# Performance work log

Hardware: AMD Instinct MI355X
Metric: run time of the kernel (lower is better)

Reference implementation:

```python
import jax, jax.numpy as jnp
import numpy as np

B, N, QD = 2, 1024, 512          # batch (ref+feat), tokens (32x32), query_dim
H, DH = 8, 64                    # heads, dim_head
INNER = H * DH
HW = 64                          # raw mask spatial size
SCALE = DH ** (-0.5)


def setup_inputs() -> dict:
    key = jax.random.key(0)
    ks = jax.random.split(key, 6)
    s = 0.02
    x = jax.random.normal(ks[0], (B, N, QD), jnp.float32)
    mask = jax.random.randint(ks[1], (B // 2, 1, HW, HW), 0, 2).astype(jnp.float32)
    Wq = jax.random.normal(ks[2], (INNER, QD), jnp.float32) * s
    Wk = jax.random.normal(ks[3], (INNER, QD), jnp.float32) * s
    Wv = jax.random.normal(ks[4], (INNER, QD), jnp.float32) * s
    # zero_module only zeroes to_out at init; use random weights for a meaningful baseline
    Wo = jax.random.normal(ks[5], (QD, INNER), jnp.float32) * s
    bo = jnp.zeros((QD,), jnp.float32)
    return {"x": x, "mask": mask, "Wq": Wq, "Wk": Wk, "Wv": Wv, "Wo": Wo, "bo": bo, "share": 1}


def nearest_resize(m, size):
    # PyTorch F.interpolate(mode='nearest'): src = floor(dst * in/out)
    ih = (jnp.arange(size) * m.shape[-2]) // size
    iw = (jnp.arange(size) * m.shape[-1]) // size
    return m[:, :, ih][:, :, :, iw]


def adain(feat, ref, mask):
    # feat, ref: (b, n, d); mask: (b, n, 1) binary
    ref_std = jnp.std(ref, axis=-2, keepdims=True, ddof=1)   # torch std is unbiased
    ref_mean = jnp.mean(ref, axis=-2, keepdims=True)
    cnt = jnp.sum(mask, axis=-2, keepdims=True)              # (b,1,1)
    f_mean = jnp.sum(feat * mask, axis=-2, keepdims=True) / cnt
    f_var = jnp.sum(mask * (feat - f_mean) ** 2, axis=-2, keepdims=True) / (cnt - 1.0)
    f_std = jnp.sqrt(f_var)
    new = (feat - f_mean) / f_std * ref_std + ref_mean
    return new * mask + feat * (1.0 - mask)


def split_heads(t):
    b, n, _ = t.shape
    return t.reshape(b, n, H, DH).transpose(0, 2, 1, 3).reshape(b * H, n, DH)


def reference(x, mask, Wq, Wk, Wv, Wo, bo, share):
    q = x @ Wq.T
    k = x @ Wk.T
    v = x @ Wv.T
    size = int(N ** 0.5)  # 32
    m = nearest_resize(mask, size).reshape(-1, N, 1)  # (B//2, N, 1)
    ref_k, feat_k = k[: B // 2], k[B // 2:]
    ref_v, feat_v = v[: B // 2], v[B // 2:]
    feat_k = adain(feat_k, ref_k, m)
    feat_v = adain(feat_v, ref_v, m)
    k = jnp.concatenate([ref_k, feat_k], axis=0)
    v = jnp.concatenate([ref_v, feat_v], axis=0)
    k = jnp.concatenate([k, jnp.tile(ref_k, (2, 1, 1))], axis=1)  # (B, 2N, INNER)
    v = jnp.concatenate([v, jnp.tile(ref_v, (2, 1, 1))], axis=1)
    qh, kh, vh = split_heads(q), split_heads(k), split_heads(v)
    sim = jnp.einsum('bid,bjd->bij', qh, kh) * SCALE  # (B*H, N, 2N)
    am = jnp.tile(m, (H, 1, N))                       # (B//2*H, N, N)
    am = (1.0 - am) * (-1e9)
    am = jnp.concatenate([jnp.zeros_like(am), am], axis=0)   # (B*H, N, N)
    am = jnp.concatenate([jnp.zeros_like(am), am], axis=-1)  # (B*H, N, 2N)
    attn = jax.nn.softmax(sim + am, axis=-1)
    out = jnp.einsum('bij,bjd->bid', attn, vh)               # (B*H, N, DH)
    out = out.reshape(B, H, N, DH).transpose(0, 2, 1, 3).reshape(B, N, INNER)
    return out @ Wo.T + bo
```

## Files before the change

### kernel.cpp

```cpp
#include <hip/hip_runtime.h>
#include <math.h>

#define NTOK 1024
#define QDIM 512
#define NH 8
#define DHD 64

using s16x8 = __attribute__((ext_vector_type(8))) short;
using f32x4 = __attribute__((ext_vector_type(4))) float;

__device__ __forceinline__ unsigned short f2bf(float x) {
  union { float f; unsigned u; } v; v.f = x;
  unsigned r = (v.u + 0x7fffu + ((v.u >> 16) & 1u)) >> 16;
  return (unsigned short)r;
}
__device__ __forceinline__ float bf2f(unsigned short h) {
  union { unsigned u; float f; } v; v.u = ((unsigned)h) << 16;
  return v.f;
}
__device__ __forceinline__ unsigned cvt_pk_bf16(float lo, float hi) {
  unsigned r;
  asm volatile("v_cvt_pk_bf16_f32 %0, %1, %2" : "=v"(r) : "v"(lo), "v"(hi));
  return r;
}

__global__ __launch_bounds__(256) void cast_kernel(
    const float* __restrict__ x, const float* __restrict__ Wq, const float* __restrict__ Wk,
    const float* __restrict__ Wv, const float* __restrict__ Wo, unsigned short* __restrict__ dst)
{
  const int tid = blockIdx.x * 256 + threadIdx.x;
  const int e = tid * 4;
  const float* src;
  if (e < 1048576) {
    src = x + e;
  } else {
    const int we = e - 1048576;
    const int wi = we >> 18;
    const int off = we & 262143;
    src = (wi == 0 ? Wq : wi == 1 ? Wk : wi == 2 ? Wv : Wo) + off;
  }
  float4 v = *(const float4*)src;
  ushort4 o;
  o.x = f2bf(v.x); o.y = f2bf(v.y); o.z = f2bf(v.z); o.w = f2bf(v.w);
  *(ushort4*)&dst[e] = o;
}

__global__ __launch_bounds__(256) void proj_mfma_kernel(
    const unsigned short* __restrict__ x_b, const unsigned short* __restrict__ w_b,
    unsigned short* __restrict__ q_b, unsigned short* __restrict__ k_b,
    unsigned short* __restrict__ v_b)
{
  const int w = threadIdx.x >> 6;
  const int l = threadIdx.x & 63;
  const int lq = l & 15, lg = l >> 4;
  const int tile = blockIdx.x * 4 + w;
  const int mat = blockIdx.y >> 3;
  const int h = blockIdx.y & 7;
  const unsigned short* W = w_b + (size_t)mat * 262144 + (size_t)(h * 64) * QDIM;
  const int tok0 = tile * 16;

  const unsigned short* xp = &x_b[(size_t)(tok0 + lq) * QDIM + lg * 8];
  const unsigned short* wp = &W[(size_t)lq * QDIM + lg * 8];

  f32x4 acc[4] = {};
  s16x8 aA, bA[4], aB, bB[4];
  aA = *(const s16x8*)&xp[0];
#pragma unroll
  for (int nf = 0; nf < 4; ++nf) bA[nf] = *(const s16x8*)&wp[(size_t)nf * 16 * QDIM];

  for (int kt = 0; kt < 16; kt += 2) {
    aB = *(const s16x8*)&xp[(kt + 1) * 32];
#pragma unroll
    for (int nf = 0; nf < 4; ++nf) bB[nf] = *(const s16x8*)&wp[(size_t)nf * 16 * QDIM + (kt + 1) * 32];
#pragma unroll
    for (int nf = 0; nf < 4; ++nf)
      acc[nf] = __builtin_amdgcn_mfma_f32_16x16x32_bf16(aA, bA[nf], acc[nf], 0, 0, 0);
    if (kt + 2 < 16) {
      aA = *(const s16x8*)&xp[(kt + 2) * 32];
#pragma unroll
      for (int nf = 0; nf < 4; ++nf) bA[nf] = *(const s16x8*)&wp[(size_t)nf * 16 * QDIM + (kt + 2) * 32];
    }
#pragma unroll
    for (int nf = 0; nf < 4; ++nf)
      acc[nf] = __builtin_amdgcn_mfma_f32_16x16x32_bf16(aB, bB[nf], acc[nf], 0, 0, 0);
  }

  const float scale = (mat == 0) ? 0.125f : 1.0f;
  unsigned short* dst = (mat == 0 ? q_b : mat == 1 ? k_b : v_b);
  const int b = tok0 >> 10;
  const int tl0 = tok0 & 1023;
  unsigned short* dp = dst + (size_t)(b * NH + h) * NTOK * DHD;
#pragma unroll
  for (int nf = 0; nf < 4; ++nf)
#pragma unroll
    for (int r = 0; r < 4; ++r)
      dp[(size_t)(tl0 + lg * 4 + r) * DHD + nf * 16 + lq] = f2bf(acc[nf][r] * scale);
}

__global__ __launch_bounds__(256) void adain_stats_kernel(
    const unsigned short* __restrict__ k_b, const unsigned short* __restrict__ v_b,
    const float* __restrict__ mask, float* __restrict__ stats_p, float* __restrict__ stats_cnt)
{
  const int id = blockIdx.x;
  const int arr = id >> 7, h = (id >> 4) & 7, ch = id & 15;
  const unsigned short* base = arr ? v_b : k_b;
  const unsigned short* refp = base + (size_t)h * 65536;
  const unsigned short* fep  = base + (size_t)(8 + h) * 65536;
  const int t = threadIdx.x, dh = t & 63, ig = t >> 6;

  if (arr == 0 && h == 0 && t < 64) {
    const int tok = ch * 64 + t;
    float c = mask[(tok >> 5) * 128 + (tok & 31) * 2];
#pragma unroll
    for (int off = 1; off < 64; off <<= 1) c += __shfl_xor(c, off);
    if (t == 0) stats_cnt[ch] = c;
  }

  float rs = 0.f, rq = 0.f, fs = 0.f, fq = 0.f;
  for (int i = 0; i < 16; ++i) {
    const int tok = ch * 64 + ig * 16 + i;
    const float rv = bf2f(refp[(size_t)tok * DHD + dh]);
    rs += rv; rq += rv * rv;
    const float fv = bf2f(fep[(size_t)tok * DHD + dh]);
    const float mm = mask[(tok >> 5) * 128 + (tok & 31) * 2];
    fs += mm * fv; fq += mm * fv * fv;
  }
  __shared__ float red[4][256];
  red[0][t] = rs; red[1][t] = rq; red[2][t] = fs; red[3][t] = fq;
  __syncthreads();
  if (ig == 0) {
    rs = red[0][dh] + red[0][dh + 64] + red[0][dh + 128] + red[0][dh + 192];
    rq = red[1][dh] + red[1][dh + 64] + red[1][dh + 128] + red[1][dh + 192];
    fs = red[2][dh] + red[2][dh + 64] + red[2][dh + 128] + red[2][dh + 192];
    fq = red[3][dh] + red[3][dh + 64] + red[3][dh + 128] + red[3][dh + 192];
    float* sp = stats_p + (size_t)id * 256;
    sp[dh] = rs; sp[64 + dh] = rq; sp[128 + dh] = fs; sp[192 + dh] = fq;
  }
}

__global__ __launch_bounds__(256) void adain_apply_kernel(
    unsigned short* __restrict__ k_b, unsigned short* __restrict__ v_b,
    const float* __restrict__ mask, const float* __restrict__ stats_p,
    const float* __restrict__ stats_cnt)
{
  const int id = blockIdx.x;
  const int arr = id >> 7, h = (id >> 4) & 7, ch = id & 15;
  unsigned short* fep = (arr ? v_b : k_b) + (size_t)(8 + h) * 65536;
  const int t = threadIdx.x, dh = t & 63, ig = t >> 6;

  __shared__ float sA[64], sB[64];
  if (t < 64) {
    float cnt = 0.f;
#pragma unroll
    for (int c = 0; c < 16; ++c) cnt += stats_cnt[c];
    const float* sp = stats_p + (size_t)((arr << 7) | (h << 4)) * 256;
    float rs = 0.f, rq = 0.f, fs = 0.f, fq = 0.f;
#pragma unroll
    for (int c = 0; c < 16; ++c) {
      rs += sp[c * 256 + t]; rq += sp[c * 256 + 64 + t];
      fs += sp[c * 256 + 128 + t]; fq += sp[c * 256 + 192 + t];
    }
    const float rmean = rs * (1.0f / 1024.0f);
    const float rstd = sqrtf(fmaxf((rq - 1024.0f * rmean * rmean) * (1.0f / 1023.0f), 0.f));
    const float fmean = fs / cnt;
    const float fstd = sqrtf(fmaxf((fq - cnt * fmean * fmean) / (cnt - 1.0f), 0.f));
    const float a = rstd / fstd;
    sA[t] = a; sB[t] = rmean - fmean * a;
  }
  __syncthreads();
  const float a = sA[dh], bb = sB[dh];
  for (int i = 0; i < 16; ++i) {
    const int tok = ch * 64 + ig * 16 + i;
    if (mask[(tok >> 5) * 128 + (tok & 31) * 2] != 0.f) {
      const float fv = bf2f(fep[(size_t)tok * DHD + dh]);
      fep[(size_t)tok * DHD + dh] = f2bf(fv * a + bb);
    }
  }
}

__global__ __launch_bounds__(256) void vtrans_kernel(const unsigned short* __restrict__ v_b,
                                                     unsigned short* __restrict__ v_bT)
{
  const int bh = blockIdx.y;
  const int tc = blockIdx.x;
  __shared__ unsigned short T[64][72];
  const int t = threadIdx.x;
  {
    const int tok = t >> 2, d0 = (t & 3) * 16;
    const unsigned short* src = v_b + ((size_t)bh * NTOK + tc * 64 + tok) * DHD + d0;
    ushort4 a0 = *(const ushort4*)&src[0];
    ushort4 a1 = *(const ushort4*)&src[4];
    ushort4 a2 = *(const ushort4*)&src[8];
    ushort4 a3 = *(const ushort4*)&src[12];
    T[d0 + 0][tok] = a0.x; T[d0 + 1][tok] = a0.y; T[d0 + 2][tok] = a0.z; T[d0 + 3][tok] = a0.w;
    T[d0 + 4][tok] = a1.x; T[d0 + 5][tok] = a1.y; T[d0 + 6][tok] = a1.z; T[d0 + 7][tok] = a1.w;
    T[d0 + 8][tok] = a2.x; T[d0 + 9][tok] = a2.y; T[d0 +10][tok] = a2.z; T[d0 +11][tok] = a2.w;
    T[d0 +12][tok] = a3.x; T[d0 +13][tok] = a3.y; T[d0 +14][tok] = a3.z; T[d0 +15][tok] = a3.w;
  }
  __syncthreads();
  {
    const int dh = t >> 2, t0 = (t & 3) * 16;
    unsigned short* dst = v_bT + ((size_t)bh * DHD + dh) * NTOK + tc * 64 + t0;
    s16x8 r0 = *(const s16x8*)&T[dh][t0];
    s16x8 r1 = *(const s16x8*)&T[dh][t0 + 8];
    *(s16x8*)&dst[0] = r0;
    *(s16x8*)&dst[8] = r1;
  }
}

__global__ __launch_bounds__(256, 4) void attn_part_kernel(
    const unsigned short* __restrict__ q_b, const unsigned short* __restrict__ k_b,
    const unsigned short* __restrict__ v_bT, const float* __restrict__ mask,
    unsigned short* __restrict__ pO, float* __restrict__ pml)
{
  const int w = threadIdx.x >> 6;
  const int unit = blockIdx.x * 4 + w;
  int b, rr;
  if (unit < 2048) { b = 1; rr = unit; } else { b = 0; rr = unit - 2048; }
  const int hh = rr >> 8;
  const int qb = (rr >> 3) & 31;
  const int s  = rr & 7;
  const int bh = b * 8 + hh;
  const int l = threadIdx.x & 63, lq = l & 15, lg = l >> 4;

  __shared__ unsigned int P_u[4][2][16][36];

  const unsigned short* qbase = q_b + ((size_t)bh * NTOK + qb * 32) * DHD;
  s16x8 qfA0 = *(const s16x8*)&qbase[(size_t)lq * DHD + lg * 8];
  s16x8 qfA1 = *(const s16x8*)&qbase[(size_t)lq * DHD + 32 + lg * 8];
  s16x8 qfB0 = *(const s16x8*)&qbase[(size_t)(16 + lq) * DHD + lg * 8];
  s16x8 qfB1 = *(const s16x8*)&qbase[(size_t)(16 + lq) * DHD + 32 + lg * 8];

  const int ntile = (b == 0) ? 2 : 4;
  const int kv0 = s * ntile * 64;
  const int inref = (b == 1 && kv0 >= NTOK) ? 1 : 0;
  const int off0 = inref ? (kv0 - NTOK) : kv0;
  const size_t base = (size_t)(inref ? hh : bh) * 65536;
  const unsigned short* kbase = k_b + base + (size_t)off0 * DHD;
  const unsigned short* vbase = v_bT + base + off0;

  float mnegA = 0.f, mnegB = 0.f;
  if (inref) {
    const int qA = qb * 32 + lq, qB = qA + 16;
    mnegA = (1.0f - mask[(qA >> 5) * 128 + (qA & 31) * 2]) * (-1e9f);
    mnegB = (1.0f - mask[(qB >> 5) * 128 + (qB & 31) * 2]) * (-1e9f);
  }

  float mrowA = -1e30f, lrowA = 0.f;
  float mrowB = -1e30f, lrowB = 0.f;
  f32x4 oA[4] = {}, oB[4] = {};

  for (int tt = 0; tt < ntile; ++tt) {
    const unsigned short* kp = kbase + (size_t)tt * 64 * DHD;
    const unsigned short* vp = vbase + tt * 64;

    f32x4 sfA[4], sfB[4];
#pragma unroll
    for (int mf = 0; mf < 4; ++mf) {
      s16x8 a0 = *(const s16x8*)&kp[(size_t)(mf * 16 + lq) * DHD + lg * 8];
      s16x8 a1 = *(const s16x8*)&kp[(size_t)(mf * 16 + lq) * DHD + 32 + lg * 8];
      f32x4 z0 = {};
      z0 = __builtin_amdgcn_mfma_f32_16x16x32_bf16(a0, qfA0, z0, 0, 0, 0);
      sfA[mf] = __builtin_amdgcn_mfma_f32_16x16x32_bf16(a1, qfA1, z0, 0, 0, 0);
      f32x4 z1 = {};
      z1 = __builtin_amdgcn_mfma_f32_16x16x32_bf16(a0, qfB0, z1, 0, 0, 0);
      sfB[mf] = __builtin_amdgcn_mfma_f32_16x16x32_bf16(a1, qfB1, z1, 0, 0, 0);
    }

    const float addA = inref ? mnegA : 0.0f;
    const float addB = inref ? mnegB : 0.0f;
    float tmA = -1e30f, tmB = -1e30f;
#pragma unroll
    for (int mf = 0; mf < 4; ++mf)
#pragma unroll
      for (int r = 0; r < 4; ++r) {
        sfA[mf][r] += addA; tmA = fmaxf(tmA, sfA[mf][r]);
        sfB[mf][r] += addB; tmB = fmaxf(tmB, sfB[mf][r]);
      }
    tmA = fmaxf(tmA, __shfl_xor(tmA, 16));
    tmA = fmaxf(tmA, __shfl_xor(tmA, 32));
    tmB = fmaxf(tmB, __shfl_xor(tmB, 16));
    tmB = fmaxf(tmB, __shfl_xor(tmB, 32));

    if (!__all(tmA <= mrowA + 8.0f)) {
      const float mnew = fmaxf(mrowA, tmA);
      const float alpha = __expf(mrowA - mnew);
      mrowA = mnew;
      lrowA *= alpha;
      float ar[4];
#pragma unroll
      for (int r = 0; r < 4; ++r) ar[r] = __shfl(alpha, lg * 4 + r, 16);
#pragma unroll
      for (int nf = 0; nf < 4; ++nf)
#pragma unroll
        for (int r = 0; r < 4; ++r) oA[nf][r] *= ar[r];
    }
    if (!__all(tmB <= mrowB + 8.0f)) {
      const float mnew = fmaxf(mrowB, tmB);
      const float alpha = __expf(mrowB - mnew);
      mrowB = mnew;
      lrowB *= alpha;
      float ar[4];
#pragma unroll
      for (int r = 0; r < 4; ++r) ar[r] = __shfl(alpha, lg * 4 + r, 16);
#pragma unroll
      for (int nf = 0; nf < 4; ++nf)
#pragma unroll
        for (int r = 0; r < 4; ++r) oB[nf][r] *= ar[r];
    }

    float pA[4][4], pB[4][4];
    float psA = 0.f, psB = 0.f;
#pragma unroll
    for (int mf = 0; mf < 4; ++mf)
#pragma unroll
      for (int r = 0; r < 4; ++r) {
        const float eA = __expf(sfA[mf][r] - mrowA); pA[mf][r] = eA; psA += eA;
        const float eB = __expf(sfB[mf][r] - mrowB); pB[mf][r] = eB; psB += eB;
      }
    psA += __shfl_xor(psA, 16);
    psA += __shfl_xor(psA, 32);
    lrowA += psA;
    psB += __shfl_xor(psB, 16);
    psB += __shfl_xor(psB, 32);
    lrowB += psB;

#pragma unroll
    for (int mf = 0; mf < 4; ++mf) {
      uint2 wa;
      wa.x = cvt_pk_bf16(pA[mf][0], pA[mf][1]);
      wa.y = cvt_pk_bf16(pA[mf][2], pA[mf][3]);
      *(uint2*)&P_u[w][0][lq][8 * mf + 2 * lg] = wa;
      uint2 wb;
      wb.x = cvt_pk_bf16(pB[mf][0], pB[mf][1]);
      wb.y = cvt_pk_bf16(pB[mf][2], pB[mf][3]);
      *(uint2*)&P_u[w][1][lq][8 * mf + 2 * lg] = wb;
    }

#pragma unroll
    for (int ks = 0; ks < 2; ++ks) {
      s16x8 paA = *(const s16x8*)&P_u[w][0][lq][16 * ks + 4 * lg];
      s16x8 paB = *(const s16x8*)&P_u[w][1][lq][16 * ks + 4 * lg];
#pragma unroll
      for (int nf = 0; nf < 4; ++nf) {
        s16x8 vb = *(const s16x8*)&vp[(size_t)(nf * 16 + lq) * NTOK + ks * 32 + lg * 8];
        oA[nf] = __builtin_amdgcn_mfma_f32_16x16x32_bf16(paA, vb, oA[nf], 0, 0, 0);
        oB[nf] = __builtin_amdgcn_mfma_f32_16x16x32_bf16(paB, vb, oB[nf], 0, 0, 0);
      }
    }
  }

  const int u = (bh * 32 + qb) * 8 + s;
  unsigned short* pop = pO + (size_t)u * 2048;
#pragma unroll
  for (int nf = 0; nf < 4; ++nf)
#pragma unroll
    for (int r = 0; r < 4; ++r) {
      pop[(size_t)(lg * 4 + r) * DHD + nf * 16 + lq] = f2bf(oA[nf][r]);
      pop[(size_t)(16 + lg * 4 + r) * DHD + nf * 16 + lq] = f2bf(oB[nf][r]);
    }
  if (l < 16) {
    pml[(size_t)u * 64 + lq] = mrowA;
    pml[(size_t)u * 64 + 16 + lq] = lrowA;
  } else if (l < 32) {
    pml[(size_t)u * 64 + 32 + lq] = mrowB;
    pml[(size_t)u * 64 + 48 + lq] = lrowB;
  }
}

__global__ __launch_bounds__(64) void attn_merge_kernel(
    const unsigned short* __restrict__ pO, const float* __restrict__ pml,
    unsigned short* __restrict__ o_b)
{
  const int id = blockIdx.x;
  const int bh = id >> 6, qt = id & 63;
  const int qb = qt >> 1, half = qt & 1;
  const int l = threadIdx.x, r = l & 15, dblk = l >> 4;
  const int d0 = dblk * 16;
  const int u0 = (bh * 32 + qb) * 8;
  const int mo = half * 32;
  const int row = half * 16 + r;

  float ms[8], ls[8];
  float M = -1e30f;
#pragma unroll
  for (int s = 0; s < 8; ++s) {
    ms[s] = pml[(size_t)(u0 + s) * 64 + mo + r];
    ls[s] = pml[(size_t)(u0 + s) * 64 + mo + 16 + r];
    M = fmaxf(M, ms[s]);
  }
  float Lsum = 0.f;
  float o[16];
#pragma unroll
  for (int j = 0; j < 16; ++j) o[j] = 0.f;
#pragma unroll
  for (int s = 0; s < 8; ++s) {
    const float alpha = __expf(ms[s] - M);
    Lsum += alpha * ls[s];
    const unsigned short* po = pO + (size_t)(u0 + s) * 2048 + (size_t)row * DHD + d0;
    s16x8 a = *(const s16x8*)&po[0];
    s16x8 c = *(const s16x8*)&po[8];
#pragma unroll
    for (int j = 0; j < 8; ++j) {
      o[j] += alpha * bf2f((unsigned short)a[j]);
      o[8 + j] += alpha * bf2f((unsigned short)c[j]);
    }
  }
  const float inv = 1.0f / Lsum;
  unsigned short* dst = o_b + ((size_t)bh * NTOK + qt * 16 + r) * DHD + d0;
  ushort4 w0, w1, w2, w3;
  w0.x = f2bf(o[0] * inv);  w0.y = f2bf(o[1] * inv);  w0.z = f2bf(o[2] * inv);  w0.w = f2bf(o[3] * inv);
  w1.x = f2bf(o[4] * inv);  w1.y = f2bf(o[5] * inv);  w1.z = f2bf(o[6] * inv);  w1.w = f2bf(o[7] * inv);
  w2.x = f2bf(o[8] * inv);  w2.y = f2bf(o[9] * inv);  w2.z = f2bf(o[10] * inv); w2.w = f2bf(o[11] * inv);
  w3.x = f2bf(o[12] * inv); w3.y = f2bf(o[13] * inv); w3.z = f2bf(o[14] * inv); w3.w = f2bf(o[15] * inv);
  *(ushort4*)&dst[0] = w0; *(ushort4*)&dst[4] = w1;
  *(ushort4*)&dst[8] = w2; *(ushort4*)&dst[12] = w3;
}

__global__ __launch_bounds__(256) void outproj_mfma_kernel(
    const unsigned short* __restrict__ o_b, const unsigned short* __restrict__ Wo_b,
    const float* __restrict__ bo, float* __restrict__ out)
{
  const int w = threadIdx.x >> 6, l = threadIdx.x & 63;
  const int lq = l & 15, lg = l >> 4;
  const int tile = blockIdx.x * 4 + w;
  const int c0 = blockIdx.y * 64;
  const int tok = tile * 16 + lq;
  const int b = tok >> 10, tl = tok & 1023;

  const unsigned short* obase = o_b + (size_t)(b * NH) * NTOK * DHD + (size_t)tl * DHD + lg * 8;
  const unsigned short* wp = &Wo_b[(size_t)(c0 + lq) * QDIM + lg * 8];

#define OP_A(KT) (*(const s16x8*)&obase[(size_t)((KT) >> 1) * NTOK * DHD + ((KT) & 1) * 32])

  f32x4 acc[4] = {};
  s16x8 aA, bA[4], aB, bB[4];
  aA = OP_A(0);
#pragma unroll
  for (int nf = 0; nf < 4; ++nf) bA[nf] = *(const s16x8*)&wp[(size_t)nf * 16 * QDIM];

  for (int kt = 0; kt < 16; kt += 2) {
    aB = OP_A(kt + 1);
#pragma unroll
    for (int nf = 0; nf < 4; ++nf) bB[nf] = *(const s16x8*)&wp[(size_t)nf * 16 * QDIM + (kt + 1) * 32];
#pragma unroll
    for (int nf = 0; nf < 4; ++nf)
      acc[nf] = __builtin_amdgcn_mfma_f32_16x16x32_bf16(aA, bA[nf], acc[nf], 0, 0, 0);
    if (kt + 2 < 16) {
      aA = OP_A(kt + 2);
#pragma unroll
      for (int nf = 0; nf < 4; ++nf) bA[nf] = *(const s16x8*)&wp[(size_t)nf * 16 * QDIM + (kt + 2) * 32];
    }
#pragma unroll
    for (int nf = 0; nf < 4; ++nf)
      acc[nf] = __builtin_amdgcn_mfma_f32_16x16x32_bf16(aB, bB[nf], acc[nf], 0, 0, 0);
  }
#undef OP_A

  const int row0 = tile * 16;
#pragma unroll
  for (int nf = 0; nf < 4; ++nf) {
    const float bv = bo[c0 + nf * 16 + lq];
#pragma unroll
    for (int r = 0; r < 4; ++r)
      out[(size_t)(row0 + lg * 4 + r) * QDIM + c0 + nf * 16 + lq] = acc[nf][r] + bv;
  }
}

extern "C" void kernel_launch(void* const* d_in, const int* in_sizes, int n_in,
                              void* d_out, int out_size, void* d_ws, size_t ws_size,
                              hipStream_t stream) {
  const float* x    = (const float*)d_in[0];
  const float* mask = (const float*)d_in[1];
  const float* Wq   = (const float*)d_in[2];
  const float* Wk   = (const float*)d_in[3];
  const float* Wv   = (const float*)d_in[4];
  const float* Wo   = (const float*)d_in[5];
  const float* bo   = (const float*)d_in[6];
  float* out = (float*)d_out;

  char* ws = (char*)d_ws;
  unsigned short* x_b  = (unsigned short*)ws;
  unsigned short* w_b  = (unsigned short*)(ws + 2097152);
  unsigned short* Wo_b = (unsigned short*)(ws + 2097152 + 3 * 524288);
  unsigned short* q_b  = (unsigned short*)(ws + 4194304);
  unsigned short* k_b  = (unsigned short*)(ws + 6291456);
  unsigned short* v_b  = (unsigned short*)(ws + 8388608);
  unsigned short* v_bT = (unsigned short*)(ws + 10485760);
  unsigned short* o_b  = (unsigned short*)(ws + 12582912);
  unsigned short* pO   = (unsigned short*)(ws + 14680064);
  float* pml       = (float*)(ws + 2097152);
  float* stats_p   = (float*)(ws + 0);
  float* stats_cnt = (float*)(ws + 262144);

  cast_kernel<<<2048, 256, 0, stream>>>(x, Wq, Wk, Wv, Wo, x_b);
  proj_mfma_kernel<<<dim3(32, 24), 256, 0, stream>>>(x_b, w_b, q_b, k_b, v_b);
  adain_stats_kernel<<<256, 256, 0, stream>>>(k_b, v_b, mask, stats_p, stats_cnt);
  adain_apply_kernel<<<256, 256, 0, stream>>>(k_b, v_b, mask, stats_p, stats_cnt);
  vtrans_kernel<<<dim3(16, 16), 256, 0, stream>>>(v_b, v_bT);
  attn_part_kernel<<<1024, 256, 0, stream>>>(q_b, k_b, v_bT, mask, pO, pml);
  attn_merge_kernel<<<1024, 64, 0, stream>>>(pO, pml, o_b);
  outproj_mfma_kernel<<<dim3(32, 8), 256, 0, stream>>>(o_b, Wo_b, bo, out);
}
```

Measured before the change: 161.0 us.

## Fuse V AdaIN apply into transpose and double token tile in projection GEMMs

The projection and output-projection MFMA kernels now compute 32 tokens per wave instead of 16, so each weight fragment is reused across two A tiles and half as many blocks are launched. The AdaIN apply for V moves into the V-transpose kernel, which recomputes the per-channel scale and shift from the partial stats and applies them before transposing. The separate apply kernel now covers only K (128 blocks), removing one full read-modify-write pass over V. The cost is more registers per wave and fewer blocks in the GEMMs, which may lower occupancy.

Result: no change. 160.0 us (-0.6%).

```diff
diff --git a/kernel.cpp b/kernel.cpp
--- a/kernel.cpp
+++ b/kernel.cpp
@@ -57,32 +57,40 @@
   const int mat = blockIdx.y >> 3;
   const int h = blockIdx.y & 7;
   const unsigned short* W = w_b + (size_t)mat * 262144 + (size_t)(h * 64) * QDIM;
-  const int tok0 = tile * 16;
-
-  const unsigned short* xp = &x_b[(size_t)(tok0 + lq) * QDIM + lg * 8];
+  const int tok0 = tile * 32;
+
+  const unsigned short* xp0 = &x_b[(size_t)(tok0 + lq) * QDIM + lg * 8];
+  const unsigned short* xp1 = &x_b[(size_t)(tok0 + 16 + lq) * QDIM + lg * 8];
   const unsigned short* wp = &W[(size_t)lq * QDIM + lg * 8];
 
-  f32x4 acc[4] = {};
-  s16x8 aA, bA[4], aB, bB[4];
-  aA = *(const s16x8*)&xp[0];
+  f32x4 acc0[4] = {}, acc1[4] = {};
+  s16x8 aA0, aA1, bA[4], aB0, aB1, bB[4];
+  aA0 = *(const s16x8*)&xp0[0];
+  aA1 = *(const s16x8*)&xp1[0];
 #pragma unroll
   for (int nf = 0; nf < 4; ++nf) bA[nf] = *(const s16x8*)&wp[(size_t)nf * 16 * QDIM];
 
   for (int kt = 0; kt < 16; kt += 2) {
-    aB = *(const s16x8*)&xp[(kt + 1) * 32];
+    aB0 = *(const s16x8*)&xp0[(kt + 1) * 32];
+    aB1 = *(const s16x8*)&xp1[(kt + 1) * 32];
 #pragma unroll
     for (int nf = 0; nf < 4; ++nf) bB[nf] = *(const s16x8*)&wp[(size_t)nf * 16 * QDIM + (kt + 1) * 32];
 #pragma unroll
-    for (int nf = 0; nf < 4; ++nf)
-      acc[nf] = __builtin_amdgcn_mfma_f32_16x16x32_bf16(aA, bA[nf], acc[nf], 0, 0, 0);
+    for (int nf = 0; nf < 4; ++nf) {
+      acc0[nf] = __builtin_amdgcn_mfma_f32_16x16x32_bf16(aA0, bA[nf], acc0[nf], 0, 0, 0);
+      acc1[nf] = __builtin_amdgcn_mfma_f32_16x16x32_bf16(aA1, bA[nf], acc1[nf], 0, 0, 0);
+    }
     if (kt + 2 < 16) {
-      aA = *(const s16x8*)&xp[(kt + 2) * 32];
+      aA0 = *(const s16x8*)&xp0[(kt + 2) * 32];
+      aA1 = *(const s16x8*)&xp1[(kt + 2) * 32];
 #pragma unroll
       for (int nf = 0; nf < 4; ++nf) bA[nf] = *(const s16x8*)&wp[(size_t)nf * 16 * QDIM + (kt + 2) * 32];
     }
 #pragma unroll
-    for (int nf = 0; nf < 4; ++nf)
-      acc[nf] = __builtin_amdgcn_mfma_f32_16x16x32_bf16(aB, bB[nf], acc[nf], 0, 0, 0);
+    for (int nf = 0; nf < 4; ++nf) {
+      acc0[nf] = __builtin_amdgcn_mfma_f32_16x16x32_bf16(aB0, bB[nf], acc0[nf], 0, 0, 0);
+      acc1[nf] = __builtin_amdgcn_mfma_f32_16x16x32_bf16(aB1, bB[nf], acc1[nf], 0, 0, 0);
+    }
   }
 
   const float scale = (mat == 0) ? 0.125f : 1.0f;
@@ -93,8 +101,10 @@
 #pragma unroll
   for (int nf = 0; nf < 4; ++nf)
 #pragma unroll
-    for (int r = 0; r < 4; ++r)
-      dp[(size_t)(tl0 + lg * 4 + r) * DHD + nf * 16 + lq] = f2bf(acc[nf][r] * scale);
+    for (int r = 0; r < 4; ++r) {
+      dp[(size_t)(tl0 + lg * 4 + r) * DHD + nf * 16 + lq] = f2bf(acc0[nf][r] * scale);
+      dp[(size_t)(tl0 + 16 + lg * 4 + r) * DHD + nf * 16 + lq] = f2bf(acc1[nf][r] * scale);
+    }
 }
 
 __global__ __launch_bounds__(256) void adain_stats_kernel(
@@ -178,24 +188,57 @@
   }
 }
 
-__global__ __launch_bounds__(256) void vtrans_kernel(const unsigned short* __restrict__ v_b,
-                                                     unsigned short* __restrict__ v_bT)
+__global__ __launch_bounds__(256) void vtrans_adain_kernel(
+    const unsigned short* __restrict__ v_b, unsigned short* __restrict__ v_bT,
+    const float* __restrict__ mask, const float* __restrict__ stats_p,
+    const float* __restrict__ stats_cnt)
 {
   const int bh = blockIdx.y;
   const int tc = blockIdx.x;
   __shared__ unsigned short T[64][72];
+  __shared__ float sA[64], sB[64];
   const int t = threadIdx.x;
+  const bool feat = (bh >= 8);
+
+  if (feat) {
+    if (t < 64) {
+      float cnt = 0.f;
+#pragma unroll
+      for (int c = 0; c < 16; ++c) cnt += stats_cnt[c];
+      const float* sp = stats_p + (size_t)(128 | ((bh - 8) << 4)) * 256;
+      float rs = 0.f, rq = 0.f, fs = 0.f, fq = 0.f;
+#pragma unroll
+      for (int c = 0; c < 16; ++c) {
+        rs += sp[c * 256 + t]; rq += sp[c * 256 + 64 + t];
+        fs += sp[c * 256 + 128 + t]; fq += sp[c * 256 + 192 + t];
+      }
+      const float rmean = rs * (1.0f / 1024.0f);
+      const float rstd = sqrtf(fmaxf((rq - 1024.0f * rmean * rmean) * (1.0f / 1023.0f), 0.f));
+      const float fmean = fs / cnt;
+      const float fstd = sqrtf(fmaxf((fq - cnt * fmean * fmean) / (cnt - 1.0f), 0.f));
+      const float a = rstd / fstd;
+      sA[t] = a; sB[t] = rmean - fmean * a;
+    }
+    __syncthreads();
+  }
+
   {
     const int tok = t >> 2, d0 = (t & 3) * 16;
-    const unsigned short* src = v_b + ((size_t)bh * NTOK + tc * 64 + tok) * DHD + d0;
+    const int gtok = tc * 64 + tok;
+    const unsigned short* src = v_b + ((size_t)bh * NTOK + gtok) * DHD + d0;
     ushort4 a0 = *(const ushort4*)&src[0];
     ushort4 a1 = *(const ushort4*)&src[4];
     ushort4 a2 = *(const ushort4*)&src[8];
     ushort4 a3 = *(const ushort4*)&src[12];
-    T[d0 + 0][tok] = a0.x; T[d0 + 1][tok] = a0.y; T[d0 + 2][tok] = a0.z; T[d0 + 3][tok] = a0.w;
-    T[d0 + 4][tok] = a1.x; T[d0 + 5][tok] = a1.y; T[d0 + 6][tok] = a1.z; T[d0 + 7][tok] = a1.w;
-    T[d0 + 8][tok] = a2.x; T[d0 + 9][tok] = a2.y; T[d0 +10][tok] = a2.z; T[d0 +11][tok] = a2.w;
-    T[d0 +12][tok] = a3.x; T[d0 +13][tok] = a3.y; T[d0 +14][tok] = a3.z; T[d0 +15][tok] = a3.w;
+    unsigned short vv[16] = {a0.x, a0.y, a0.z, a0.w, a1.x, a1.y, a1.z, a1.w,
+                             a2.x, a2.y, a2.z, a2.w, a3.x, a3.y, a3.z, a3.w};
+    if (feat && mask[(gtok >> 5) * 128 + (gtok & 31) * 2] != 0.f) {
+#pragma unroll
+      for (int j = 0; j < 16; ++j)
+        vv[j] = f2bf(bf2f(vv[j]) * sA[d0 + j] + sB[d0 + j]);
+    }
+#pragma unroll
+    for (int j = 0; j < 16; ++j) T[d0 + j][tok] = vv[j];
   }
   __syncthreads();
   {
@@ -425,45 +468,57 @@
   const int lq = l & 15, lg = l >> 4;
   const int tile = blockIdx.x * 4 + w;
   const int c0 = blockIdx.y * 64;
-  const int tok = tile * 16 + lq;
-  const int b = tok >> 10, tl = tok & 1023;
-
-  const unsigned short* obase = o_b + (size_t)(b * NH) * NTOK * DHD + (size_t)tl * DHD + lg * 8;
+  const int tok0 = tile * 32;
+  const int b = tok0 >> 10, tl0 = tok0 & 1023;
+
+  const unsigned short* obase0 = o_b + (size_t)(b * NH) * NTOK * DHD + (size_t)(tl0 + lq) * DHD + lg * 8;
+  const unsigned short* obase1 = o_b + (size_t)(b * NH) * NTOK * DHD + (size_t)(tl0 + 16 + lq) * DHD + lg * 8;
   const unsigned short* wp = &Wo_b[(size_t)(c0 + lq) * QDIM + lg * 8];
 
-#define OP_A(KT) (*(const s16x8*)&obase[(size_t)((KT) >> 1) * NTOK * DHD + ((KT) & 1) * 32])
-
-  f32x4 acc[4] = {};
-  s16x8 aA, bA[4], aB, bB[4];
-  aA = OP_A(0);
+#define OP_A0(KT) (*(const s16x8*)&obase0[(size_t)((KT) >> 1) * NTOK * DHD + ((KT) & 1) * 32])
+#define OP_A1(KT) (*(const s16x8*)&obase1[(size_t)((KT) >> 1) * NTOK * DHD + ((KT) & 1) * 32])
+
+  f32x4 acc0[4] = {}, acc1[4] = {};
+  s16x8 aA0, aA1, bA[4], aB0, aB1, bB[4];
+  aA0 = OP_A0(0);
+  aA1 = OP_A1(0);
 #pragma unroll
   for (int nf = 0; nf < 4; ++nf) bA[nf] = *(const s16x8*)&wp[(size_t)nf * 16 * QDIM];
 
   for (int kt = 0; kt < 16; kt += 2) {
-    aB = OP_A(kt + 1);
+    aB0 = OP_A0(kt + 1);
+    aB1 = OP_A1(kt + 1);
 #pragma unroll
     for (int nf = 0; nf < 4; ++nf) bB[nf] = *(const s16x8*)&wp[(size_t)nf * 16 * QDIM + (kt + 1) * 32];
 #pragma unroll
-    for (int nf = 0; nf < 4; ++nf)
-      acc[nf] = __builtin_amdgcn_mfma_f32_16x16x32_bf16(aA, bA[nf], acc[nf], 0, 0, 0);
+    for (int nf = 0; nf < 4; ++nf) {
+      acc0[nf] = __builtin_amdgcn_mfma_f32_16x16x32_bf16(aA0, bA[nf], acc0[nf], 0, 0, 0);
+      acc1[nf] = __builtin_amdgcn_mfma_f32_16x16x32_bf16(aA1, bA[nf], acc1[nf], 0, 0, 0);
+    }
     if (kt + 2 < 16) {
-      aA = OP_A(kt + 2);
+      aA0 = OP_A0(kt + 2);
+      aA1 = OP_A1(kt + 2);
 #pragma unroll
       for (int nf = 0; nf < 4; ++nf) bA[nf] = *(const s16x8*)&wp[(size_t)nf * 16 * QDIM + (kt + 2) * 32];
     }
 #pragma unroll
-    for (int nf = 0; nf < 4; ++nf)
-      acc[nf] = __builtin_amdgcn_mfma_f32_16x16x32_bf16(aB, bB[nf], acc[nf], 0, 0, 0);
-  }
-#undef OP_A
-
-  const int row0 = tile * 16;
+    for (int nf = 0; nf < 4; ++nf) {
+      acc0[nf] = __builtin_amdgcn_mfma_f32_16x16x32_bf16(aB0, bB[nf], acc0[nf], 0, 0, 0);
+      acc1[nf] = __builtin_amdgcn_mfma_f32_16x16x32_bf16(aB1, bB[nf], acc1[nf], 0, 0, 0);
+    }
+  }
+#undef OP_A0
+#undef OP_A1
+
+  const int row0 = tile * 32;
 #pragma unroll
   for (int nf = 0; nf < 4; ++nf) {
     const float bv = bo[c0 + nf * 16 + lq];
 #pragma unroll
-    for (int r = 0; r < 4; ++r)
-      out[(size_t)(row0 + lg * 4 + r) * QDIM + c0 + nf * 16 + lq] = acc[nf][r] + bv;
+    for (int r = 0; r < 4; ++r) {
+      out[(size_t)(row0 + lg * 4 + r) * QDIM + c0 + nf * 16 + lq] = acc0[nf][r] + bv;
+      out[(size_t)(row0 + 16 + lg * 4 + r) * QDIM + c0 + nf * 16 + lq] = acc1[nf][r] + bv;
+    }
   }
 }
 
@@ -494,11 +549,11 @@
   float* stats_cnt = (float*)(ws + 262144);
 
   cast_kernel<<<2048, 256, 0, stream>>>(x, Wq, Wk, Wv, Wo, x_b);
-  proj_mfma_kernel<<<dim3(32, 24), 256, 0, stream>>>(x_b, w_b, q_b, k_b, v_b);
+  proj_mfma_kernel<<<dim3(16, 24), 256, 0, stream>>>(x_b, w_b, q_b, k_b, v_b);
   adain_stats_kernel<<<256, 256, 0, stream>>>(k_b, v_b, mask, stats_p, stats_cnt);
-  adain_apply_kernel<<<256, 256, 0, stream>>>(k_b, v_b, mask, stats_p, stats_cnt);
-  vtrans_kernel<<<dim3(16, 16), 256, 0, stream>>>(v_b, v_bT);
+  adain_apply_kernel<<<128, 256, 0, stream>>>(k_b, v_b, mask, stats_p, stats_cnt);
+  vtrans_adain_kernel<<<dim3(16, 16), 256, 0, stream>>>(v_b, v_bT, mask, stats_p, stats_cnt);
   attn_part_kernel<<<1024, 256, 0, stream>>>(q_b, k_b, v_bT, mask, pO, pml);
   attn_merge_kernel<<<1024, 64, 0, stream>>>(pO, pml, o_b);
-  outproj_mfma_kernel<<<dim3(32, 8), 256, 0, stream>>>(o_b, Wo_b, bo, out);
-}
+  outproj_mfma_kernel<<<dim3(16, 8), 256, 0, stream>>>(o_b, Wo_b, bo, out);
+}
```
